# Performance work log

Hardware: AMD Instinct MI355X
Metric: run time of the kernel (lower is better)

Reference implementation:

```python
import jax, jax.numpy as jnp
import numpy as np

N = 50000      # nodes
E = 1600000    # edges (before self loops)
B = 512        # graphs
D = 128        # gcn dim (constant across the 3 GAT layers)
H = 1024       # hidden_dim
O = 128        # output_dim
NEG_SLOPE = 0.2


def setup_inputs() -> dict:
    key = jax.random.key(0)
    ks = jax.random.split(key, 24)
    inp = {
        "x": jax.random.normal(ks[0], (N, D), jnp.float32),
        "edge_index": jax.random.randint(ks[1], (2, E), 0, N, dtype=jnp.int64),
        "edge_weight": jax.random.uniform(ks[2], (E,), jnp.float32),
        "batch": jnp.sort(jax.random.randint(ks[3], (N,), 0, B, dtype=jnp.int64)),
    }
    s = 1.0 / np.sqrt(D)
    for i in range(3):
        k = 4 + 4 * i
        inp[f"W{i+1}"] = jax.random.normal(ks[k], (D, D), jnp.float32) * s
        inp[f"as{i+1}"] = jax.random.normal(ks[k + 1], (D,), jnp.float32) * s
        inp[f"ad{i+1}"] = jax.random.normal(ks[k + 2], (D,), jnp.float32) * s
        inp[f"b{i+1}"] = jnp.zeros((D,), jnp.float32)
    inp["Wf1"] = jax.random.normal(ks[16], (D, H), jnp.float32) * s
    inp["bf1"] = jnp.zeros((H,), jnp.float32)
    inp["Wf2"] = jax.random.normal(ks[17], (H, O), jnp.float32) * (1.0 / np.sqrt(H))
    inp["bf2"] = jnp.zeros((O,), jnp.float32)
    return inp


def gat_conv(x, src, dst, W, a_src, a_dst, b):
    """PyG GATConv, heads=1: gather -> leakyrelu -> segment softmax -> scatter-add."""
    h = x @ W                                   # [N, D]
    e = jax.nn.leaky_relu(jnp.take(h @ a_src, src) + jnp.take(h @ a_dst, dst), NEG_SLOPE)  # [E']
    m = jax.ops.segment_max(e, dst, num_segments=N)
    ex = jnp.exp(e - m[dst])
    denom = jax.ops.segment_sum(ex, dst, num_segments=N)
    alpha = ex / denom[dst]                      # segment softmax over incoming edges
    out = jax.ops.segment_sum(alpha[:, None] * h[src], dst, num_segments=N)
    return out + b


def reference(x, edge_index, edge_weight, batch,
              W1, as1, ad1, b1, W2, as2, ad2, b2, W3, as3, ad3, b3,
              Wf1, bf1, Wf2, bf2):
    # GATConv adds self loops; edge_weight is unused by GATConv (faithful to original)
    loop = jnp.arange(N, dtype=edge_index.dtype)
    src = jnp.concatenate([edge_index[0], loop])
    dst = jnp.concatenate([edge_index[1], loop])

    h = gat_conv(x, src, dst, W1, as1, ad1, b1)
    h = jax.nn.relu(gat_conv(h, src, dst, W2, as2, ad2, b2))
    h = jax.nn.relu(gat_conv(h, src, dst, W3, as3, ad3, b3))

    # global mean pool (gep)
    sums = jax.ops.segment_sum(h, batch, num_segments=B)        # [B, D]
    counts = jax.ops.segment_sum(jnp.ones((N,), h.dtype), batch, num_segments=B)
    pooled = sums / jnp.maximum(counts, 1.0)[:, None]

    # MLP head; dropout is identity at inference
    o = jax.nn.relu(pooled) @ Wf1 + bf1
    o = jax.nn.relu(o) @ Wf2 + bf2
    return o
```

## Files before the change

### kernel.cpp

```cpp
#include <hip/hip_runtime.h>
#include <cstdint>
#include <cstddef>

#define NEG_SLOPE 0.2f

typedef _Float16 f16x8 __attribute__((ext_vector_type(8)));
typedef float f32x4v __attribute__((ext_vector_type(4)));

__device__ __forceinline__ unsigned enc_f(float f) {
  unsigned u = __float_as_uint(f);
  return (u & 0x80000000u) ? ~u : (u | 0x80000000u);
}
__device__ __forceinline__ float dec_f(unsigned u) {
  return (u & 0x80000000u) ? __uint_as_float(u ^ 0x80000000u) : __uint_as_float(~u);
}

#define AST 136
#define ABYTES (64 * AST * 2)
#define SMEM_BYTES (ABYTES + 4 * 64 * 2 * 4)

__global__ void k_bounds_prep(const int* __restrict__ batch, int N, int B,
                              int* __restrict__ gstart, unsigned* __restrict__ maxPart,
                              int* __restrict__ counts,
                              const float* __restrict__ W1, const float* __restrict__ W2,
                              const float* __restrict__ W3,
                              _Float16* __restrict__ Wt1, _Float16* __restrict__ Wt2,
                              _Float16* __restrict__ Wt3, int nbb) {
  int b = blockIdx.x;
  if (b >= nbb) {
    int wi = b - nbb;
    const float* W = (wi == 0) ? W1 : (wi == 1) ? W2 : W3;
    _Float16* Wt = (wi == 0) ? Wt1 : (wi == 1) ? Wt2 : Wt3;
    for (int i = threadIdx.x; i < 2048; i += 256) {
      int k = i >> 4, n8 = (i & 15) << 3;
      float4 v0 = *(const float4*)&W[(size_t)k * 128 + n8];
      float4 v1 = *(const float4*)&W[(size_t)k * 128 + n8 + 4];
      Wt[(size_t)(n8 + 0) * 128 + k] = (_Float16)v0.x;
      Wt[(size_t)(n8 + 1) * 128 + k] = (_Float16)v0.y;
      Wt[(size_t)(n8 + 2) * 128 + k] = (_Float16)v0.z;
      Wt[(size_t)(n8 + 3) * 128 + k] = (_Float16)v0.w;
      Wt[(size_t)(n8 + 4) * 128 + k] = (_Float16)v1.x;
      Wt[(size_t)(n8 + 5) * 128 + k] = (_Float16)v1.y;
      Wt[(size_t)(n8 + 6) * 128 + k] = (_Float16)v1.z;
      Wt[(size_t)(n8 + 7) * 128 + k] = (_Float16)v1.w;
    }
    return;
  }
  int n = b * blockDim.x + threadIdx.x;
  if (n < 768) maxPart[n] = 0u;
  if (n >= N) return;
  counts[n] = 0;
  int cur = batch[n];
  if (n == 0) {
    for (int g = 0; g <= cur; g++) gstart[g] = 0;
  } else {
    int prev = batch[n - 1];
    for (int g = prev + 1; g <= cur; g++) gstart[g] = n;
  }
  if (n == N - 1) {
    for (int g = cur + 1; g <= B; g++) gstart[g] = N;
  }
}

__global__ __launch_bounds__(1024) void k_scan1(const int* __restrict__ counts, int N,
                                                int* __restrict__ row_ptr, int* __restrict__ part) {
  __shared__ int tmp[1024];
  int t = threadIdx.x;
  int i = blockIdx.x * 1024 + t;
  int v = (i < N) ? 1 + counts[i] : 0;
  tmp[t] = v;
  __syncthreads();
  for (int off = 1; off < 1024; off <<= 1) {
    int u = (t >= off) ? tmp[t - off] : 0;
    __syncthreads();
    tmp[t] += u;
    __syncthreads();
  }
  if (i < N) row_ptr[i + 1] = tmp[t];
  if (t == 1023) part[blockIdx.x] = tmp[t];
}

__global__ __launch_bounds__(1024) void k_scan3(int* __restrict__ row_ptr,
                                                const int* __restrict__ part, int N) {
  __shared__ int s_off;
  int bi = blockIdx.x;
  if (threadIdx.x == 0) {
    int run = 0;
    for (int b = 0; b < bi; b++) run += part[b];
    s_off = run;
    if (bi == 0) row_ptr[0] = 0;
  }
  __syncthreads();
  int i = bi * 1024 + threadIdx.x;
  if (i < N) row_ptr[i + 1] += s_off;
}

__device__ __forceinline__ void gemm_body(char* smem, int bx,
                                          const float* __restrict__ A32,
                                          const unsigned short* __restrict__ A16,
                                          const _Float16* __restrict__ WtG,
                                          unsigned short* __restrict__ hb,
                                          const float* __restrict__ asrc,
                                          const float* __restrict__ adst,
                                          float* __restrict__ sv, float* __restrict__ dv,
                                          unsigned* __restrict__ maxSlot, int M) {
  _Float16* Ah = (_Float16*)smem;
  float (*sred)[64][2] = (float (*)[64][2])(smem + ABYTES);
  int t = threadIdx.x;
  int rowbase = bx * 64;

  if (A16) {
    for (int i = t; i < 64 * 16; i += 256) {
      int r = i >> 4, c8 = (i & 15) << 3;
      int gr = rowbase + r;
      uint4 v = make_uint4(0u, 0u, 0u, 0u);
      if (gr < M) v = *(const uint4*)&A16[(size_t)gr * 128 + c8];
      *(uint4*)&Ah[r * AST + c8] = v;
    }
  } else {
    for (int i = t; i < 64 * 32; i += 256) {
      int r = i >> 5, c4 = (i & 31) << 2;
      int gr = rowbase + r;
      float4 v = make_float4(0.f, 0.f, 0.f, 0.f);
      if (gr < M) v = *(const float4*)&A32[(size_t)gr * 128 + c4];
      _Float16 tmp[4] = {(_Float16)v.x, (_Float16)v.y, (_Float16)v.z, (_Float16)v.w};
      *(short4*)&Ah[r * AST + c4] = *(short4*)tmp;
    }
  }
  __syncthreads();

  int wave = t >> 6, lane = t & 63, quad = lane >> 4, l15 = lane & 15;
  f32x4v acc[4][2];
#pragma unroll
  for (int mt = 0; mt < 4; mt++)
#pragma unroll
    for (int nt = 0; nt < 2; nt++) {
      acc[mt][nt][0] = 0.f; acc[mt][nt][1] = 0.f; acc[mt][nt][2] = 0.f; acc[mt][nt][3] = 0.f;
    }

#pragma unroll
  for (int s = 0; s < 4; s++) {
    int k0 = (s << 5) + (quad << 3);
    f16x8 af[4], bf[2];
#pragma unroll
    for (int mt = 0; mt < 4; mt++)
      af[mt] = *(f16x8*)&Ah[(mt * 16 + l15) * AST + k0];
#pragma unroll
    for (int nt = 0; nt < 2; nt++)
      bf[nt] = *(const f16x8*)&WtG[(size_t)(wave * 32 + nt * 16 + l15) * 128 + k0];
#pragma unroll
    for (int mt = 0; mt < 4; mt++)
#pragma unroll
      for (int nt = 0; nt < 2; nt++)
        acc[mt][nt] = __builtin_amdgcn_mfma_f32_16x16x32_f16(af[mt], bf[nt], acc[mt][nt], 0, 0, 0);
  }
  __syncthreads();

  float avv0 = asrc[wave * 32 + l15],      avv1 = asrc[wave * 32 + 16 + l15];
  float adv0 = adst[wave * 32 + l15],      adv1 = adst[wave * 32 + 16 + l15];
  _Float16* hS16 = (_Float16*)smem;
#pragma unroll
  for (int mt = 0; mt < 4; mt++) {
#pragma unroll
    for (int rr = 0; rr < 4; rr++) {
      int row = mt * 16 + quad * 4 + rr;
      hS16[row * AST + wave * 32 + l15]      = (_Float16)acc[mt][0][rr];
      hS16[row * AST + wave * 32 + 16 + l15] = (_Float16)acc[mt][1][rr];
      float ps = acc[mt][0][rr] * avv0 + acc[mt][1][rr] * avv1;
      float pd = acc[mt][0][rr] * adv0 + acc[mt][1][rr] * adv1;
#pragma unroll
      for (int mask = 8; mask; mask >>= 1) {
        ps += __shfl_xor(ps, mask);
        pd += __shfl_xor(pd, mask);
      }
      if (l15 == 0) { sred[wave][row][0] = ps; sred[wave][row][1] = pd; }
    }
  }
  __syncthreads();

  int tx = t & 31, ty = t >> 5;
#pragma unroll
  for (int r8 = 0; r8 < 8; r8++) {
    int row = r8 * 8 + ty;
    int gr = rowbase + row;
    if (gr < M)
      *(uint2*)&hb[(size_t)gr * 128 + tx * 4] = *(const uint2*)&hS16[row * AST + tx * 4];
  }

  if (t < 64) {
    int gr = rowbase + t;
    float ps = sred[0][t][0] + sred[1][t][0] + sred[2][t][0] + sred[3][t][0];
    float pd = sred[0][t][1] + sred[1][t][1] + sred[2][t][1] + sred[3][t][1];
    float wmax = -1e30f;
    if (gr < M) { sv[gr] = ps; dv[gr] = pd; wmax = ps; }
#pragma unroll
    for (int mask = 32; mask; mask >>= 1) wmax = fmaxf(wmax, __shfl_xor(wmax, mask));
    if (t == 0) atomicMax(&maxSlot[bx & 255], enc_f(wmax));
  }
}

__global__ __launch_bounds__(256) void k_count_gemm(const int* __restrict__ dst, int E,
                                                    int* counts, int* __restrict__ rank,
                                                    const float* __restrict__ A32,
                                                    const _Float16* __restrict__ WtG,
                                                    unsigned short* __restrict__ hb,
                                                    const float* __restrict__ asrc,
                                                    const float* __restrict__ adst,
                                                    float* __restrict__ sv, float* __restrict__ dv,
                                                    unsigned* __restrict__ maxSlot, int Gg, int N) {
  __shared__ __align__(16) char smem[SMEM_BYTES];
  int b = (int)blockIdx.x;
  bool isGemm = ((b & 7) == 4) && ((b >> 3) < Gg);
  if (isGemm) {
    gemm_body(smem, b >> 3, A32, (const unsigned short*)nullptr, WtG,
              hb, asrc, adst, sv, dv, maxSlot, N);
  } else {
    int nGemmBefore = (b >= 4) ? min(((b - 4) >> 3) + 1, Gg) : 0;
    int e = (b - nGemmBefore) * 256 + threadIdx.x;
    if (e < E) rank[e] = atomicAdd(&counts[dst[e]], 1);
  }
}

__global__ __launch_bounds__(256) void k_fill(const int* __restrict__ src,
                                              const int* __restrict__ dst,
                                              const int* __restrict__ rank, int E, int N,
                                              const int* __restrict__ row_ptr,
                                              int* __restrict__ col) {
  int i = blockIdx.x * 256 + threadIdx.x;
  if (i < N) col[row_ptr[i]] = i;
  int e = i - N;
  if (e >= 0 && e < E) col[row_ptr[dst[e]] + 1 + rank[e]] = src[e];
}

__global__ __launch_bounds__(256) void k_gemm_fused(const unsigned short* __restrict__ A16,
                                                    const _Float16* __restrict__ WtG,
                                                    unsigned short* __restrict__ hb,
                                                    const float* __restrict__ asrc,
                                                    const float* __restrict__ adst,
                                                    float* __restrict__ sv, float* __restrict__ dv,
                                                    unsigned* __restrict__ maxSlot, int M) {
  __shared__ __align__(16) char smem[SMEM_BYTES];
  gemm_body(smem, (int)blockIdx.x, (const float*)nullptr, A16, WtG,
            hb, asrc, adst, sv, dv, maxSlot, M);
}

__global__ __launch_bounds__(256) void k_agg(const unsigned short* __restrict__ hb,
                                             const float* __restrict__ sv,
                                             const float* __restrict__ dv,
                                             const int* __restrict__ row_ptr,
                                             const int* __restrict__ col,
                                             const float* __restrict__ bias,
                                             const unsigned* __restrict__ maxSlot,
                                             unsigned short* __restrict__ out16,
                                             int N, int relu) {
  int wid = (int)((blockIdx.x * (size_t)blockDim.x + threadIdx.x) >> 6);
  int lane = threadIdx.x & 63;
  if (wid >= N) return;

  unsigned mp = max(max(maxSlot[lane], maxSlot[lane + 64]),
                    max(maxSlot[lane + 128], maxSlot[lane + 192]));
#pragma unroll
  for (int off = 32; off; off >>= 1) mp = max(mp, __shfl_xor(mp, off));
  float maxS = dec_f(mp);

  int beg = row_ptr[wid], end = row_ptr[wid + 1];
  float dn = dv[wid];
  float m = maxS + dn;
  m = (m > 0.f) ? m : NEG_SLOPE * m;

  int g = lane >> 4, sub = lane & 15;
  const uint32_t* hbu = (const uint32_t*)hb;
  float acc[8];
#pragma unroll
  for (int k = 0; k < 8; k++) acc[k] = 0.f;
  float dsum = 0.f;

#define FETCH_SLOT(K, W, H)                                                \
  {                                                                        \
    int sl = ((K) << 2) + g;                                               \
    int sn = __shfl(sn_l, sl);                                             \
    W = __shfl(w_l, sl);                                                   \
    H = make_uint4(0u, 0u, 0u, 0u);                                        \
    if (sl < cnt) H = *(const uint4*)(hbu + (size_t)sn * 64 + sub * 4);    \
  }
#define ACC_SLOT(W, H)                                                     \
  {                                                                        \
    const _Float16* hp = (const _Float16*)&H;                              \
    _Pragma("unroll")                                                      \
    for (int q = 0; q < 8; q++) acc[q] += W * (float)hp[q];                \
  }

  for (int base = beg; base < end; base += 64) {
    int cnt = min(end - base, 64);

    int sn_l = 0;
    float w_l = 0.f;
    if (lane < cnt) {
      sn_l = col[base + lane];
      float e = sv[sn_l] + dn;
      e = (e > 0.f) ? e : NEG_SLOPE * e;
      w_l = __expf(e - m);
      dsum += w_l;
    }

    int kmaxW = (cnt + 3) >> 2;
    float wA, wB, wC, wD, wE, wF;
    uint4 hA, hB, hC, hD, hE, hF;
    FETCH_SLOT(0, wA, hA);
    FETCH_SLOT(1, wB, hB);
    FETCH_SLOT(2, wC, hC);
    FETCH_SLOT(3, wD, hD);
    FETCH_SLOT(4, wE, hE);
    for (int k = 5; k < kmaxW; k++) {
      FETCH_SLOT(k, wF, hF);
      ACC_SLOT(wA, hA);
      wA = wB; hA = hB;
      wB = wC; hB = hC;
      wC = wD; hC = hD;
      wD = wE; hD = hE;
      wE = wF; hE = hF;
    }
    ACC_SLOT(wA, hA);
    ACC_SLOT(wB, hB);
    ACC_SLOT(wC, hC);
    ACC_SLOT(wD, hD);
    ACC_SLOT(wE, hE);
  }

#pragma unroll
  for (int off = 1; off < 64; off <<= 1) dsum += __shfl_xor(dsum, off);
#pragma unroll
  for (int k = 0; k < 8; k++) {
    acc[k] += __shfl_xor(acc[k], 16);
    acc[k] += __shfl_xor(acc[k], 32);
  }
  if (lane < 16) {
    float inv = 1.f / dsum;
    float o[8];
    const float* bp = &bias[sub * 8];
#pragma unroll
    for (int k = 0; k < 8; k++) {
      o[k] = acc[k] * inv + bp[k];
      if (relu) o[k] = fmaxf(o[k], 0.f);
    }
    _Float16 q[8];
#pragma unroll
    for (int k = 0; k < 8; k++) q[k] = (_Float16)o[k];
    *(uint4*)&out16[(size_t)wid * 128 + sub * 8] = *(uint4*)q;
  }
}

__global__ __launch_bounds__(256) void k_pool(const unsigned short* __restrict__ h16,
                                              const int* __restrict__ gstart,
                                              float* __restrict__ pooled, int B) {
  __shared__ float red[4][128];
  int b = blockIdx.x, t = threadIdx.x;
  int c = t & 63, seg = t >> 6;
  int s0 = gstart[b], s1 = gstart[b + 1];
  int cnt = s1 - s0;
  int per = (cnt + 3) >> 2;
  int n0 = s0 + seg * per;
  int n1 = min(n0 + per, s1);
  const uint32_t* hu = (const uint32_t*)h16;
  float a0 = 0.f, a1 = 0.f;
  for (int n = n0; n < n1; n++) {
    union { uint32_t u; _Float16 h[2]; } cv;
    cv.u = hu[(size_t)n * 64 + c];
    a0 += (float)cv.h[0];
    a1 += (float)cv.h[1];
  }
  if (seg) { red[seg][2 * c] = a0; red[seg][2 * c + 1] = a1; }
  __syncthreads();
  if (seg == 0) {
    a0 += red[1][2 * c] + red[2][2 * c] + red[3][2 * c];
    a1 += red[1][2 * c + 1] + red[2][2 * c + 1] + red[3][2 * c + 1];
    float inv = 1.f / (float)(cnt > 0 ? cnt : 1);
    pooled[b * 128 + 2 * c]     = fmaxf(a0 * inv, 0.f);
    pooled[b * 128 + 2 * c + 1] = fmaxf(a1 * inv, 0.f);
  }
}

__global__ __launch_bounds__(256) void k_mlp(const float* __restrict__ pooled,
                                             const float* __restrict__ Wf1,
                                             const float* __restrict__ bf1,
                                             const float* __restrict__ Wf2,
                                             const float* __restrict__ bf2,
                                             float* __restrict__ out, int B) {
  __shared__ float P[4][128];
  __shared__ float H1[4][1024];
  __shared__ float R[4][128];
  int t = threadIdx.x;
  int g0 = blockIdx.x * 4;

  for (int i = t; i < 4 * 128; i += 256) {
    int gi = i >> 7, c = i & 127;
    P[gi][c] = (g0 + gi < B) ? pooled[(size_t)(g0 + gi) * 128 + c] : 0.f;
  }
  __syncthreads();

#pragma unroll
  for (int cb = 0; cb < 4; cb++) {
    int c = cb * 256 + t;
    float a0 = 0.f, a1 = 0.f, a2 = 0.f, a3 = 0.f;
    for (int k = 0; k < 128; k++) {
      float w = Wf1[(size_t)k * 1024 + c];
      a0 += P[0][k] * w; a1 += P[1][k] * w; a2 += P[2][k] * w; a3 += P[3][k] * w;
    }
    float b = bf1[c];
    H1[0][c] = fmaxf(a0 + b, 0.f);
    H1[1][c] = fmaxf(a1 + b, 0.f);
    H1[2][c] = fmaxf(a2 + b, 0.f);
    H1[3][c] = fmaxf(a3 + b, 0.f);
  }
  __syncthreads();

  int c = t & 127, hh = t >> 7;
  float a0 = 0.f, a1 = 0.f, a2 = 0.f, a3 = 0.f;
  int k0 = hh * 512;
  for (int k = k0; k < k0 + 512; k++) {
    float w = Wf2[(size_t)k * 128 + c];
    a0 += H1[0][k] * w; a1 += H1[1][k] * w; a2 += H1[2][k] * w; a3 += H1[3][k] * w;
  }
  if (hh == 1) { R[0][c] = a0; R[1][c] = a1; R[2][c] = a2; R[3][c] = a3; }
  __syncthreads();
  if (hh == 0) {
    float b = bf2[c];
    float o0 = a0 + R[0][c] + b;
    float o1 = a1 + R[1][c] + b;
    float o2 = a2 + R[2][c] + b;
    float o3 = a3 + R[3][c] + b;
    if (g0 + 0 < B) out[(size_t)(g0 + 0) * 128 + c] = o0;
    if (g0 + 1 < B) out[(size_t)(g0 + 1) * 128 + c] = o1;
    if (g0 + 2 < B) out[(size_t)(g0 + 2) * 128 + c] = o2;
    if (g0 + 3 < B) out[(size_t)(g0 + 3) * 128 + c] = o3;
  }
}

extern "C" void kernel_launch(void* const* d_in, const int* in_sizes, int n_in,
                              void* d_out, int out_size, void* d_ws, size_t ws_size,
                              hipStream_t stream) {
  const float* x     = (const float*)d_in[0];
  const int*   ei    = (const int*)d_in[1];
  const int*   batch = (const int*)d_in[3];
  const float* W1 = (const float*)d_in[4];
  const float* as1 = (const float*)d_in[5];
  const float* ad1 = (const float*)d_in[6];
  const float* b1 = (const float*)d_in[7];
  const float* W2 = (const float*)d_in[8];
  const float* as2 = (const float*)d_in[9];
  const float* ad2 = (const float*)d_in[10];
  const float* b2 = (const float*)d_in[11];
  const float* W3 = (const float*)d_in[12];
  const float* as3 = (const float*)d_in[13];
  const float* ad3 = (const float*)d_in[14];
  const float* b3 = (const float*)d_in[15];
  const float* Wf1 = (const float*)d_in[16];
  const float* bf1 = (const float*)d_in[17];
  const float* Wf2 = (const float*)d_in[18];
  const float* bf2 = (const float*)d_in[19];

  const int N = in_sizes[0] / 128;
  const int E = in_sizes[1] / 2;
  const int B = out_size / 128;

  char* base_ws = (char*)d_ws;
  size_t off = 0;
  auto carve = [&](size_t bytes) -> void* {
    off = (off + 255) & ~(size_t)255;
    void* p = base_ws + off;
    off += bytes;
    return p;
  };
  int* counts   = (int*)carve((size_t)N * 4);
  int* row_ptr  = (int*)carve((size_t)(N + 1) * 4);
  int* rank     = (int*)carve((size_t)E * 4);
  int* col      = (int*)carve((size_t)(E + N) * 4);
  int* part     = (int*)carve(1024 * 4);
  int* gstart   = (int*)carve((size_t)(B + 1) * 4);
  unsigned* maxPart = (unsigned*)carve(768 * 4);
  float* sbuf   = (float*)carve((size_t)N * 4);
  float* dbuf   = (float*)carve((size_t)N * 4);
  unsigned short* hb  = (unsigned short*)carve((size_t)N * 128 * 2);
  unsigned short* a16 = (unsigned short*)carve((size_t)N * 128 * 2);
  float* pooled = (float*)carve((size_t)B * 128 * 4);
  _Float16* Wt1 = (_Float16*)carve(128 * 128 * 2);
  _Float16* Wt2 = (_Float16*)carve(128 * 128 * 2);
  _Float16* Wt3 = (_Float16*)carve(128 * 128 * 2);

  const int* srcp = ei;
  const int* dstp = ei + E;
  const int nb = (N + 1023) / 1024;
  const int Gg = (N + 63) / 64;
  const int Cb = (E + 255) / 256;
  const int Gf = (E + N + 255) / 256;
  const int nbb = (N + 255) / 256;

  hipLaunchKernelGGL(k_bounds_prep, dim3(nbb + 3), dim3(256), 0, stream,
                     batch, N, B, gstart, maxPart, counts,
                     W1, W2, W3, Wt1, Wt2, Wt3, nbb);

  hipLaunchKernelGGL(k_count_gemm, dim3(Cb + Gg), dim3(256), 0, stream,
                     dstp, E, counts, rank,
                     x, Wt1, hb, as1, ad1, sbuf, dbuf, maxPart + 0 * 256, Gg, N);

  hipLaunchKernelGGL(k_scan1, dim3(nb), dim3(1024), 0, stream, counts, N, row_ptr, part);
  hipLaunchKernelGGL(k_scan3, dim3(nb), dim3(1024), 0, stream, row_ptr, part, N);

  hipLaunchKernelGGL(k_fill, dim3(Gf), dim3(256), 0, stream,
                     srcp, dstp, rank, E, N, row_ptr, col);

  hipLaunchKernelGGL(k_agg, dim3((N + 3) / 4), dim3(256), 0, stream,
                     hb, sbuf, dbuf, row_ptr, col, b1, maxPart + 0 * 256, a16, N, 0);

  hipLaunchKernelGGL(k_gemm_fused, dim3(Gg), dim3(256), 0, stream,
                     a16, Wt2, hb, as2, ad2, sbuf, dbuf, maxPart + 1 * 256, N);
  hipLaunchKernelGGL(k_agg, dim3((N + 3) / 4), dim3(256), 0, stream,
                     hb, sbuf, dbuf, row_ptr, col, b2, maxPart + 1 * 256, a16, N, 1);

  hipLaunchKernelGGL(k_gemm_fused, dim3(Gg), dim3(256), 0, stream,
                     a16, Wt3, hb, as3, ad3, sbuf, dbuf, maxPart + 2 * 256, N);
  hipLaunchKernelGGL(k_agg, dim3((N + 3) / 4), dim3(256), 0, stream,
                     hb, sbuf, dbuf, row_ptr, col, b3, maxPart + 2 * 256, a16, N, 1);

  hipLaunchKernelGGL(k_pool, dim3(B), dim3(256), 0, stream, a16, gstart, pooled, B);
  hipLaunchKernelGGL(k_mlp, dim3((B + 3) / 4), dim3(256), 0, stream,
                     pooled, Wf1, bf1, Wf2, bf2, (float*)d_out, B);
}
```

Before: 525.6 us.

## Move layer-1 GEMM into fill kernel, split count pass, fuse pool with MLP

The layer-1 GEMM blocks now ride alongside the CSR fill kernel, interleaved one in nine, instead of alongside the atomic count pass. The count/rank pass becomes its own kernel, launched as two half-range launches. Mean pooling is folded into the MLP kernel, so each block pools its four graphs itself and the intermediate pooled buffer and one launch go away. The fused pool loop runs with only 128 blocks, which lowers the parallelism of the pooling step. Splitting the count pass adds an extra launch.

```diff
diff --git a/kernel.cpp b/kernel.cpp
--- a/kernel.cpp
+++ b/kernel.cpp
@@ -62,6 +62,12 @@
   }
 }
 
+__global__ void k_count_rank(const int* __restrict__ dst, int e0, int e1,
+                             int* counts, int* __restrict__ rank) {
+  int e = e0 + blockIdx.x * blockDim.x + threadIdx.x;
+  if (e < e1) rank[e] = atomicAdd(&counts[dst[e]], 1);
+}
+
 __global__ __launch_bounds__(1024) void k_scan1(const int* __restrict__ counts, int N,
                                                 int* __restrict__ row_ptr, int* __restrict__ part) {
   __shared__ int tmp[1024];
@@ -199,37 +205,31 @@
   }
 }
 
-__global__ __launch_bounds__(256) void k_count_gemm(const int* __restrict__ dst, int E,
-                                                    int* counts, int* __restrict__ rank,
-                                                    const float* __restrict__ A32,
-                                                    const _Float16* __restrict__ WtG,
-                                                    unsigned short* __restrict__ hb,
-                                                    const float* __restrict__ asrc,
-                                                    const float* __restrict__ adst,
-                                                    float* __restrict__ sv, float* __restrict__ dv,
-                                                    unsigned* __restrict__ maxSlot, int Gg, int N) {
+__global__ __launch_bounds__(256) void k_fill_gemm(const int* __restrict__ src,
+                                                   const int* __restrict__ dst,
+                                                   const int* __restrict__ rank, int E, int N,
+                                                   const int* __restrict__ row_ptr,
+                                                   int* __restrict__ col,
+                                                   const float* __restrict__ A32,
+                                                   const _Float16* __restrict__ WtG,
+                                                   unsigned short* __restrict__ hb,
+                                                   const float* __restrict__ asrc,
+                                                   const float* __restrict__ adst,
+                                                   float* __restrict__ sv, float* __restrict__ dv,
+                                                   unsigned* __restrict__ maxSlot, int Gg) {
   __shared__ __align__(16) char smem[SMEM_BYTES];
   int b = (int)blockIdx.x;
-  bool isGemm = ((b & 7) == 4) && ((b >> 3) < Gg);
+  bool isGemm = ((b % 9) == 4) && ((b / 9) < Gg);
   if (isGemm) {
-    gemm_body(smem, b >> 3, A32, (const unsigned short*)nullptr, WtG,
+    gemm_body(smem, b / 9, A32, (const unsigned short*)nullptr, WtG,
               hb, asrc, adst, sv, dv, maxSlot, N);
   } else {
-    int nGemmBefore = (b >= 4) ? min(((b - 4) >> 3) + 1, Gg) : 0;
-    int e = (b - nGemmBefore) * 256 + threadIdx.x;
-    if (e < E) rank[e] = atomicAdd(&counts[dst[e]], 1);
-  }
-}
-
-__global__ __launch_bounds__(256) void k_fill(const int* __restrict__ src,
-                                              const int* __restrict__ dst,
-                                              const int* __restrict__ rank, int E, int N,
-                                              const int* __restrict__ row_ptr,
-                                              int* __restrict__ col) {
-  int i = blockIdx.x * 256 + threadIdx.x;
-  if (i < N) col[row_ptr[i]] = i;
-  int e = i - N;
-  if (e >= 0 && e < E) col[row_ptr[dst[e]] + 1 + rank[e]] = src[e];
+    int nGemmBefore = (b >= 4) ? min((b - 4) / 9 + 1, Gg) : 0;
+    int i = (b - nGemmBefore) * 256 + threadIdx.x;
+    if (i < N) col[row_ptr[i]] = i;
+    int e = i - N;
+    if (e >= 0 && e < E) col[row_ptr[dst[e]] + 1 + rank[e]] = src[e];
+  }
 }
 
 __global__ __launch_bounds__(256) void k_gemm_fused(const unsigned short* __restrict__ A16,
@@ -350,89 +350,86 @@
   }
 }
 
-__global__ __launch_bounds__(256) void k_pool(const unsigned short* __restrict__ h16,
-                                              const int* __restrict__ gstart,
-                                              float* __restrict__ pooled, int B) {
-  __shared__ float red[4][128];
-  int b = blockIdx.x, t = threadIdx.x;
-  int c = t & 63, seg = t >> 6;
-  int s0 = gstart[b], s1 = gstart[b + 1];
-  int cnt = s1 - s0;
-  int per = (cnt + 3) >> 2;
-  int n0 = s0 + seg * per;
-  int n1 = min(n0 + per, s1);
-  const uint32_t* hu = (const uint32_t*)h16;
-  float a0 = 0.f, a1 = 0.f;
-  for (int n = n0; n < n1; n++) {
-    union { uint32_t u; _Float16 h[2]; } cv;
-    cv.u = hu[(size_t)n * 64 + c];
-    a0 += (float)cv.h[0];
-    a1 += (float)cv.h[1];
-  }
-  if (seg) { red[seg][2 * c] = a0; red[seg][2 * c + 1] = a1; }
-  __syncthreads();
-  if (seg == 0) {
-    a0 += red[1][2 * c] + red[2][2 * c] + red[3][2 * c];
-    a1 += red[1][2 * c + 1] + red[2][2 * c + 1] + red[3][2 * c + 1];
-    float inv = 1.f / (float)(cnt > 0 ? cnt : 1);
-    pooled[b * 128 + 2 * c]     = fmaxf(a0 * inv, 0.f);
-    pooled[b * 128 + 2 * c + 1] = fmaxf(a1 * inv, 0.f);
-  }
-}
-
-__global__ __launch_bounds__(256) void k_mlp(const float* __restrict__ pooled,
-                                             const float* __restrict__ Wf1,
-                                             const float* __restrict__ bf1,
-                                             const float* __restrict__ Wf2,
-                                             const float* __restrict__ bf2,
-                                             float* __restrict__ out, int B) {
+__global__ __launch_bounds__(256) void k_pool_mlp(const unsigned short* __restrict__ h16,
+                                                  const int* __restrict__ gstart,
+                                                  const float* __restrict__ Wf1,
+                                                  const float* __restrict__ bf1,
+                                                  const float* __restrict__ Wf2,
+                                                  const float* __restrict__ bf2,
+                                                  float* __restrict__ out, int B) {
   __shared__ float P[4][128];
   __shared__ float H1[4][1024];
   __shared__ float R[4][128];
+  __shared__ float red[4][128];
   int t = threadIdx.x;
   int g0 = blockIdx.x * 4;
-
-  for (int i = t; i < 4 * 128; i += 256) {
-    int gi = i >> 7, c = i & 127;
-    P[gi][c] = (g0 + gi < B) ? pooled[(size_t)(g0 + gi) * 128 + c] : 0.f;
-  }
-  __syncthreads();
+  int c = t & 63, seg = t >> 6;
+  const uint32_t* hu = (const uint32_t*)h16;
+
+  for (int gi = 0; gi < 4; gi++) {
+    int b = g0 + gi;
+    float a0 = 0.f, a1 = 0.f;
+    int cnt = 0;
+    if (b < B) {
+      int s0 = gstart[b], s1 = gstart[b + 1];
+      cnt = s1 - s0;
+      int per = (cnt + 3) >> 2;
+      int n0 = s0 + seg * per;
+      int n1 = min(n0 + per, s1);
+      for (int n = n0; n < n1; n++) {
+        union { uint32_t u; _Float16 h[2]; } cv;
+        cv.u = hu[(size_t)n * 64 + c];
+        a0 += (float)cv.h[0];
+        a1 += (float)cv.h[1];
+      }
+    }
+    if (seg) { red[seg][2 * c] = a0; red[seg][2 * c + 1] = a1; }
+    __syncthreads();
+    if (seg == 0) {
+      a0 += red[1][2 * c] + red[2][2 * c] + red[3][2 * c];
+      a1 += red[1][2 * c + 1] + red[2][2 * c + 1] + red[3][2 * c + 1];
+      float inv = 1.f / (float)(cnt > 0 ? cnt : 1);
+      P[gi][2 * c]     = fmaxf(a0 * inv, 0.f);
+      P[gi][2 * c + 1] = fmaxf(a1 * inv, 0.f);
+    }
+    __syncthreads();
+  }
 
 #pragma unroll
   for (int cb = 0; cb < 4; cb++) {
-    int c = cb * 256 + t;
+    int cc = cb * 256 + t;
     float a0 = 0.f, a1 = 0.f, a2 = 0.f, a3 = 0.f;
     for (int k = 0; k < 128; k++) {
-      float w = Wf1[(size_t)k * 1024 + c];
+      float w = Wf1[(size_t)k * 1024 + cc];
       a0 += P[0][k] * w; a1 += P[1][k] * w; a2 += P[2][k] * w; a3 += P[3][k] * w;
     }
-    float b = bf1[c];
-    H1[0][c] = fmaxf(a0 + b, 0.f);
-    H1[1][c] = fmaxf(a1 + b, 0.f);
-    H1[2][c] = fmaxf(a2 + b, 0.f);
-    H1[3][c] = fmaxf(a3 + b, 0.f);
-  }
-  __syncthreads();
-
-  int c = t & 127, hh = t >> 7;
+    float b = bf1[cc];
+    H1[0][cc] = fmaxf(a0 + b, 0.f);
+    H1[1][cc] = fmaxf(a1 + b, 0.f);
+    H1[2][cc] = fmaxf(a2 + b, 0.f);
+    H1[3][cc] = fmaxf(a3 + b, 0.f);
+  }
+  __syncthreads();
+
+  int cc = t & 127, hh = t >> 7;
   float a0 = 0.f, a1 = 0.f, a2 = 0.f, a3 = 0.f;
   int k0 = hh * 512;
   for (int k = k0; k < k0 + 512; k++) {
-    float w = Wf2[(size_t)k * 128 + c];
+    float w = Wf2[(size_t)k * 128 + cc];
     a0 += H1[0][k] * w; a1 += H1[1][k] * w; a2 += H1[2][k] * w; a3 += H1[3][k] * w;
   }
-  if (hh == 1) { R[0][c] = a0; R[1][c] = a1; R[2][c] = a2; R[3][c] = a3; }
+  if (hh == 1) { R[0][cc] = a0; R[1][cc] = a1; R[2][cc] = a2; R[3][cc] = a3; }
   __syncthreads();
   if (hh == 0) {
-    float b = bf2[c];
-    float o0 = a0 + R[0][c] + b;
-    float o1 = a1 + R[1][c] + b;
-    float o2 = a2 + R[2][c] + b;
-    float o3 = a3 + R[3][c] + b;
-    if (g0 + 0 < B) out[(size_t)(g0 + 0) * 128 + c] = o0;
-    if (g0 + 1 < B) out[(size_t)(g0 + 1) * 128 + c] = o1;
-    if (g0 + 2 < B) out[(size_t)(g0 + 2) * 128 + c] = o2;
-    if (g0 + 3 < B) out[(size_t)(g0 + 3) * 128 + c] = o3;
+    float b = bf2[cc];
+    float o0 = a0 + R[0][cc] + b;
+    float o1 = a1 + R[1][cc] + b;
+    float o2 = a2 + R[2][cc] + b;
+    float o3 = a3 + R[3][cc] + b;
+    if (g0 + 0 < B) out[(size_t)(g0 + 0) * 128 + cc] = o0;
+    if (g0 + 1 < B) out[(size_t)(g0 + 1) * 128 + cc] = o1;
+    if (g0 + 2 < B) out[(size_t)(g0 + 2) * 128 + cc] = o2;
+    if (g0 + 3 < B) out[(size_t)(g0 + 3) * 128 + cc] = o3;
   }
 }
 
@@ -482,7 +479,6 @@
   float* dbuf   = (float*)carve((size_t)N * 4);
   unsigned short* hb  = (unsigned short*)carve((size_t)N * 128 * 2);
   unsigned short* a16 = (unsigned short*)carve((size_t)N * 128 * 2);
-  float* pooled = (float*)carve((size_t)B * 128 * 4);
   _Float16* Wt1 = (_Float16*)carve(128 * 128 * 2);
   _Float16* Wt2 = (_Float16*)carve(128 * 128 * 2);
   _Float16* Wt3 = (_Float16*)carve(128 * 128 * 2);
@@ -491,23 +487,23 @@
   const int* dstp = ei + E;
   const int nb = (N + 1023) / 1024;
   const int Gg = (N + 63) / 64;
-  const int Cb = (E + 255) / 256;
   const int Gf = (E + N + 255) / 256;
   const int nbb = (N + 255) / 256;
+  const int Eh = E / 2;
 
   hipLaunchKernelGGL(k_bounds_prep, dim3(nbb + 3), dim3(256), 0, stream,
                      batch, N, B, gstart, maxPart, counts,
                      W1, W2, W3, Wt1, Wt2, Wt3, nbb);
-
-  hipLaunchKernelGGL(k_count_gemm, dim3(Cb + Gg), dim3(256), 0, stream,
-                     dstp, E, counts, rank,
-                     x, Wt1, hb, as1, ad1, sbuf, dbuf, maxPart + 0 * 256, Gg, N);
-
+  hipLaunchKernelGGL(k_count_rank, dim3((Eh + 255) / 256), dim3(256), 0, stream,
+                     dstp, 0, Eh, counts, rank);
+  hipLaunchKernelGGL(k_count_rank, dim3((E - Eh + 255) / 256), dim3(256), 0, stream,
+                     dstp, Eh, E, counts, rank);
   hipLaunchKernelGGL(k_scan1, dim3(nb), dim3(1024), 0, stream, counts, N, row_ptr, part);
   hipLaunchKernelGGL(k_scan3, dim3(nb), dim3(1024), 0, stream, row_ptr, part, N);
 
-  hipLaunchKernelGGL(k_fill, dim3(Gf), dim3(256), 0, stream,
-                     srcp, dstp, rank, E, N, row_ptr, col);
+  hipLaunchKernelGGL(k_fill_gemm, dim3(Gf + Gg), dim3(256), 0, stream,
+                     srcp, dstp, rank, E, N, row_ptr, col,
+                     x, Wt1, hb, as1, ad1, sbuf, dbuf, maxPart + 0 * 256, Gg);
 
   hipLaunchKernelGGL(k_agg, dim3((N + 3) / 4), dim3(256), 0, stream,
                      hb, sbuf, dbuf, row_ptr, col, b1, maxPart + 0 * 256, a16, N, 0);
@@ -522,7 +518,6 @@
   hipLaunchKernelGGL(k_agg, dim3((N + 3) / 4), dim3(256), 0, stream,
                      hb, sbuf, dbuf, row_ptr, col, b3, maxPart + 2 * 256, a16, N, 1);
 
-  hipLaunchKernelGGL(k_pool, dim3(B), dim3(256), 0, stream, a16, gstart, pooled, B);
-  hipLaunchKernelGGL(k_mlp, dim3((B + 3) / 4), dim3(256), 0, stream,
-                     pooled, Wf1, bf1, Wf2, bf2, (float*)d_out, B);
-}
+  hipLaunchKernelGGL(k_pool_mlp, dim3((B + 3) / 4), dim3(256), 0, stream,
+                     a16, gstart, Wf1, bf1, Wf2, bf2, (float*)d_out, B);
+}
```

Measured after the change: 558.7 us. 1.06x slower.

## Move layer-1 GEMM from count kernel into fill kernel and split counting

Applied to the files above, without the earlier changes.

The first-layer GEMM blocks, which were interleaved with the edge-counting atomics, are now interleaved with the CSR fill scatter at a 1-in-9 ratio. Edge counting becomes a standalone kernel launched as two halves. The aim is to take the GEMM off the atomic-heavy counting pass and hide it behind the fill pass instead. This adds one kernel launch and uses div/mod by 9 for block indexing.

```diff
diff --git a/kernel.cpp b/kernel.cpp
--- a/kernel.cpp
+++ b/kernel.cpp
@@ -62,6 +62,12 @@
   }
 }
 
+__global__ void k_count_rank(const int* __restrict__ dst, int e0, int e1,
+                             int* counts, int* __restrict__ rank) {
+  int e = e0 + blockIdx.x * blockDim.x + threadIdx.x;
+  if (e < e1) rank[e] = atomicAdd(&counts[dst[e]], 1);
+}
+
 __global__ __launch_bounds__(1024) void k_scan1(const int* __restrict__ counts, int N,
                                                 int* __restrict__ row_ptr, int* __restrict__ part) {
   __shared__ int tmp[1024];
@@ -199,37 +205,31 @@
   }
 }
 
-__global__ __launch_bounds__(256) void k_count_gemm(const int* __restrict__ dst, int E,
-                                                    int* counts, int* __restrict__ rank,
-                                                    const float* __restrict__ A32,
-                                                    const _Float16* __restrict__ WtG,
-                                                    unsigned short* __restrict__ hb,
-                                                    const float* __restrict__ asrc,
-                                                    const float* __restrict__ adst,
-                                                    float* __restrict__ sv, float* __restrict__ dv,
-                                                    unsigned* __restrict__ maxSlot, int Gg, int N) {
+__global__ __launch_bounds__(256) void k_fill_gemm(const int* __restrict__ src,
+                                                   const int* __restrict__ dst,
+                                                   const int* __restrict__ rank, int E, int N,
+                                                   const int* __restrict__ row_ptr,
+                                                   int* __restrict__ col,
+                                                   const float* __restrict__ A32,
+                                                   const _Float16* __restrict__ WtG,
+                                                   unsigned short* __restrict__ hb,
+                                                   const float* __restrict__ asrc,
+                                                   const float* __restrict__ adst,
+                                                   float* __restrict__ sv, float* __restrict__ dv,
+                                                   unsigned* __restrict__ maxSlot, int Gg) {
   __shared__ __align__(16) char smem[SMEM_BYTES];
   int b = (int)blockIdx.x;
-  bool isGemm = ((b & 7) == 4) && ((b >> 3) < Gg);
+  bool isGemm = ((b % 9) == 4) && ((b / 9) < Gg);
   if (isGemm) {
-    gemm_body(smem, b >> 3, A32, (const unsigned short*)nullptr, WtG,
+    gemm_body(smem, b / 9, A32, (const unsigned short*)nullptr, WtG,
               hb, asrc, adst, sv, dv, maxSlot, N);
   } else {
-    int nGemmBefore = (b >= 4) ? min(((b - 4) >> 3) + 1, Gg) : 0;
-    int e = (b - nGemmBefore) * 256 + threadIdx.x;
-    if (e < E) rank[e] = atomicAdd(&counts[dst[e]], 1);
-  }
-}
-
-__global__ __launch_bounds__(256) void k_fill(const int* __restrict__ src,
-                                              const int* __restrict__ dst,
-                                              const int* __restrict__ rank, int E, int N,
-                                              const int* __restrict__ row_ptr,
-                                              int* __restrict__ col) {
-  int i = blockIdx.x * 256 + threadIdx.x;
-  if (i < N) col[row_ptr[i]] = i;
-  int e = i - N;
-  if (e >= 0 && e < E) col[row_ptr[dst[e]] + 1 + rank[e]] = src[e];
+    int nGemmBefore = (b >= 4) ? min((b - 4) / 9 + 1, Gg) : 0;
+    int i = (b - nGemmBefore) * 256 + threadIdx.x;
+    if (i < N) col[row_ptr[i]] = i;
+    int e = i - N;
+    if (e >= 0 && e < E) col[row_ptr[dst[e]] + 1 + rank[e]] = src[e];
+  }
 }
 
 __global__ __launch_bounds__(256) void k_gemm_fused(const unsigned short* __restrict__ A16,
@@ -491,23 +491,23 @@
   const int* dstp = ei + E;
   const int nb = (N + 1023) / 1024;
   const int Gg = (N + 63) / 64;
-  const int Cb = (E + 255) / 256;
   const int Gf = (E + N + 255) / 256;
   const int nbb = (N + 255) / 256;
+  const int Eh = E / 2;
 
   hipLaunchKernelGGL(k_bounds_prep, dim3(nbb + 3), dim3(256), 0, stream,
                      batch, N, B, gstart, maxPart, counts,
                      W1, W2, W3, Wt1, Wt2, Wt3, nbb);
-
-  hipLaunchKernelGGL(k_count_gemm, dim3(Cb + Gg), dim3(256), 0, stream,
-                     dstp, E, counts, rank,
-                     x, Wt1, hb, as1, ad1, sbuf, dbuf, maxPart + 0 * 256, Gg, N);
-
+  hipLaunchKernelGGL(k_count_rank, dim3((Eh + 255) / 256), dim3(256), 0, stream,
+                     dstp, 0, Eh, counts, rank);
+  hipLaunchKernelGGL(k_count_rank, dim3((E - Eh + 255) / 256), dim3(256), 0, stream,
+                     dstp, Eh, E, counts, rank);
   hipLaunchKernelGGL(k_scan1, dim3(nb), dim3(1024), 0, stream, counts, N, row_ptr, part);
   hipLaunchKernelGGL(k_scan3, dim3(nb), dim3(1024), 0, stream, row_ptr, part, N);
 
-  hipLaunchKernelGGL(k_fill, dim3(Gf), dim3(256), 0, stream,
-                     srcp, dstp, rank, E, N, row_ptr, col);
+  hipLaunchKernelGGL(k_fill_gemm, dim3(Gf + Gg), dim3(256), 0, stream,
+                     srcp, dstp, rank, E, N, row_ptr, col,
+                     x, Wt1, hb, as1, ad1, sbuf, dbuf, maxPart + 0 * 256, Gg);
 
   hipLaunchKernelGGL(k_agg, dim3((N + 3) / 4), dim3(256), 0, stream,
                      hb, sbuf, dbuf, row_ptr, col, b1, maxPart + 0 * 256, a16, N, 0);
```

New measurement: 524.7 us. Within noise of the previous version (-0.2%).
